# Optimization experiments

Hardware: AMD Instinct MI355X
Metric: run time of the kernel (lower is better)

Reference implementation:

```python
import jax, jax.numpy as jnp
import numpy as np

B, L, D, V, C = 16384, 50, 128, 91718, 11
H, HD, F = 4, 32, 6
NP = F * (F - 1) // 2  # 15 pairs
CIN = F * D + NP * D   # 2688


def setup_inputs() -> dict:
    key = jax.random.key(0)
    ks = jax.random.split(key, 32)
    inp = {}
    inp['item_id'] = jax.random.randint(ks[0], (B,), 0, V)
    inp['item_mm'] = jax.random.normal(ks[1], (B, D), dtype=jnp.float32)
    inp['likes'] = jax.random.randint(ks[2], (B,), 0, C)
    inp['views'] = jax.random.randint(ks[3], (B,), 0, C)
    inp['item_seq'] = jax.random.randint(ks[4], (B, L), 0, V)
    g = lambda k, shape, s: (jax.random.normal(k, shape, dtype=jnp.float32) * s)
    inp['item_emb'] = g(ks[5], (V, D), 0.02).at[0].set(0.0)  # padding_idx=0
    inp['cate_emb'] = g(ks[6], (C, D), 0.02)
    inp['mm_w'] = g(ks[7], (D, D), (2.0 / D) ** 0.5)
    inp['mm_b'] = jnp.zeros((D,), jnp.float32)
    inp['ln_g'] = jnp.ones((D,), jnp.float32)
    inp['ln_b'] = jnp.zeros((D,), jnp.float32)
    inp['gnn_W'] = g(ks[8], (H, D, HD), (2.0 / (D + HD)) ** 0.5 * 1.414)
    inp['gnn_a'] = g(ks[9], (H, 2 * HD, 1), 0.1)
    inp['se_w1'] = g(ks[10], (F, F // 2), 0.4)
    inp['se_b1'] = jnp.zeros((F // 2,), jnp.float32)
    inp['se_w2'] = g(ks[11], (F // 2, F), 0.4)
    inp['se_b2'] = jnp.zeros((F,), jnp.float32)
    inp['bi_W'] = g(ks[12], (F - 1, D, D), (2.0 / (2 * D)) ** 0.5)
    inp['mlp_w1'] = g(ks[13], (CIN, 512), (2.0 / CIN) ** 0.5)
    inp['mlp_b1'] = jnp.zeros((512,), jnp.float32)
    inp['bn1_g'] = jnp.ones((512,), jnp.float32)
    inp['bn1_b'] = jnp.zeros((512,), jnp.float32)
    inp['mlp_w2'] = g(ks[14], (512, 256), (2.0 / 512) ** 0.5)
    inp['mlp_b2'] = jnp.zeros((256,), jnp.float32)
    inp['bn2_g'] = jnp.ones((256,), jnp.float32)
    inp['bn2_b'] = jnp.zeros((256,), jnp.float32)
    inp['mlp_w3'] = g(ks[15], (256, 1), (2.0 / 256) ** 0.5)
    inp['mlp_b3'] = jnp.zeros((1,), jnp.float32)
    return inp


def _forward(item_id, item_mm, likes, views, item_seq,
             item_emb, cate_emb, mm_w, mm_b, ln_g, ln_b,
             gnn_W, gnn_a, se_w1, se_b1, se_w2, se_b2, bi_W,
             mlp_w1, mlp_b1, bn1_g, bn1_b, mlp_w2, mlp_b2, bn2_g, bn2_b,
             mlp_w3, mlp_b3):
    bsz = item_id.shape[0]
    eps = 1e-5

    user_feat = jnp.zeros((bsz, D), item_mm.dtype)
    like_feat = cate_emb[likes]
    view_feat = cate_emb[views]
    id_feat = item_emb[item_id]

    # mm_proj: Linear -> LayerNorm -> GELU (exact)
    y = item_mm @ mm_w + mm_b
    mu = y.mean(-1, keepdims=True)
    var = y.var(-1, keepdims=True)
    y = (y - mu) * jax.lax.rsqrt(var + eps) * ln_g + ln_b
    img_feat = jax.nn.gelu(y, approximate=False)

    # masked mean pooling of history
    seq_emb = item_emb[item_seq]                          # [B,L,D]
    mask = item_seq == 0
    seq_emb = jnp.where(mask[..., None], 0.0, seq_emb)
    cnt = jnp.clip(jnp.sum((~mask).astype(seq_emb.dtype), axis=1, keepdims=True), 1.0)
    hist_feat = seq_emb.sum(1) / cnt

    x = jnp.stack([user_feat, like_feat, view_feat, id_feat, img_feat, hist_feat], axis=1)  # [B,6,D]

    # GAT over 6-node fully-connected feature graph
    hp = jnp.einsum('bni,hio->bnho', x, gnn_W)            # [B,6,H,HD]
    a1 = gnn_a[:, :HD, 0]                                  # [H,HD]
    a2 = gnn_a[:, HD:, 0]
    ei = jnp.einsum('bnhd,hd->bhn', hp, a1)
    ej = jnp.einsum('bnhd,hd->bhn', hp, a2)
    e = ei[:, :, :, None] + ej[:, :, None, :]             # [B,H,6,6]
    e = jnp.where(e > 0, e, 0.2 * e)                       # LeakyReLU(0.2)
    att = jax.nn.softmax(e, axis=-1)                       # dropout off (eval)
    h_new = jnp.einsum('bhnm,bmho->bnho', att, hp).reshape(bsz, F, D)
    gnn_feat = jax.nn.elu(h_new + x)                       # in_dim == out_dim

    # SENet
    z = gnn_feat.mean(-1)                                  # [B,6]
    w = jax.nn.sigmoid(jax.nn.relu(z @ se_w1 + se_b1) @ se_w2 + se_b2)
    s = gnn_feat * w[..., None]

    # Bilinear ('each'): vid_i = s_i @ W_i, pairs (i,j), j>i
    vid = jnp.einsum('bfd,fde->bfe', s[:, :F - 1], bi_W)   # [B,5,D]
    p = jnp.stack([vid[:, i] * s[:, j] for i in range(F - 1) for j in range(i + 1, F)], axis=1)  # [B,15,D]

    c = jnp.concatenate([gnn_feat.reshape(bsz, -1), p.reshape(bsz, -1)], axis=1)  # [B,2688]

    # MLP with eval-mode BatchNorm (running mean 0, var 1) and dropout off
    bn = lambda t, g_, b_: t * (g_ / jnp.sqrt(1.0 + eps)) + b_
    h1 = jax.nn.gelu(bn(c @ mlp_w1 + mlp_b1, bn1_g, bn1_b), approximate=False)
    h2 = jax.nn.gelu(bn(h1 @ mlp_w2 + mlp_b2, bn2_g, bn2_b), approximate=False)
    out = jax.nn.sigmoid(h2 @ mlp_w3 + mlp_b3)
    return out.squeeze(-1)


def reference(item_id, item_mm, likes, views, item_seq,
              item_emb, cate_emb, mm_w, mm_b, ln_g, ln_b,
              gnn_W, gnn_a, se_w1, se_b1, se_w2, se_b2, bi_W,
              mlp_w1, mlp_b1, bn1_g, bn1_b, mlp_w2, mlp_b2, bn2_g, bn2_b,
              mlp_w3, mlp_b3):
    return _forward(item_id, item_mm, likes, views, item_seq,
                    item_emb, cate_emb, mm_w, mm_b, ln_g, ln_b,
                    gnn_W, gnn_a, se_w1, se_b1, se_w2, se_b2, bi_W,
                    mlp_w1, mlp_b1, bn1_g, bn1_b, mlp_w2, mlp_b2, bn2_g, bn2_b,
                    mlp_w3, mlp_b3)
```

## Files before the change

### kernel.cpp

```cpp
#include <hip/hip_runtime.h>
#include <hip/hip_bf16.h>
#include <cstdint>
#include <cstddef>

#define BB 16384

typedef float  floatx4 __attribute__((ext_vector_type(4)));
typedef float  floatx2 __attribute__((ext_vector_type(2)));
typedef __bf16 bf16x8  __attribute__((ext_vector_type(8)));

__device__ __forceinline__ unsigned short f2bf(float f) {
  union { float f; unsigned int u; } v; v.f = f;
  unsigned int r = v.u + 0x7FFFu + ((v.u >> 16) & 1u);
  return (unsigned short)(r >> 16);
}
__device__ __forceinline__ float bf2f(unsigned short h) {
  union { unsigned int u; float f; } v; v.u = ((unsigned int)h) << 16;
  return v.f;
}
__device__ __forceinline__ float gelu_exact(float x) {
  return 0.5f * x * (1.0f + erff(x * 0.7071067811865475f));
}
__device__ __forceinline__ void fp8x8_to_f32(uint2 v, float* o) {
  floatx2 p0 = __builtin_amdgcn_cvt_pk_f32_fp8((int)v.x, false);
  floatx2 p1 = __builtin_amdgcn_cvt_pk_f32_fp8((int)v.x, true);
  floatx2 p2 = __builtin_amdgcn_cvt_pk_f32_fp8((int)v.y, false);
  floatx2 p3 = __builtin_amdgcn_cvt_pk_f32_fp8((int)v.y, true);
  o[0] = p0.x; o[1] = p0.y; o[2] = p1.x; o[3] = p1.y;
  o[4] = p2.x; o[5] = p2.y; o[6] = p3.x; o[7] = p3.y;
}

#define ALOAD16(g, l) \
  __builtin_amdgcn_global_load_lds((const __attribute__((address_space(1))) void*)(g), \
                                   (__attribute__((address_space(3))) void*)(l), 16, 0, 0)

__global__ __launch_bounds__(256)
void k_prep(const float* __restrict__ gnn_W, const float* __restrict__ gnn_a,
            const float* __restrict__ item_mm, const float* __restrict__ item_emb,
            const float* __restrict__ w1, const float* __restrict__ w2,
            const float* __restrict__ bi_W, const float* __restrict__ mm_w,
            unsigned short* __restrict__ wallt2, unsigned short* __restrict__ immb,
            unsigned char* __restrict__ iembf8,
            unsigned short* __restrict__ w1t, unsigned short* __restrict__ w2t,
            unsigned short* __restrict__ biwt, unsigned short* __restrict__ mmwt)
{
  __shared__ float tile[64][65];
  if (blockIdx.x < 2048) {
    const int total = 18432 + 524288 + 1467488;
    for (int id = blockIdx.x * 256 + threadIdx.x; id < total; id += 2048 * 256) {
      if (id < 18432) {
        int n = id / 128, k = id % 128;
        if (n < 128) {
          wallt2[id] = f2bf(gnn_W[(n >> 5) * 4096 + k * 32 + (n & 31)]);
        } else if (n < 136) {
          int h = (n - 128) & 3;
          int off = (n < 132) ? 0 : 32;
          float s = 0.f;
          for (int o = 0; o < 32; o++)
            s += gnn_W[h * 4096 + k * 32 + o] * gnn_a[h * 64 + off + o];
          wallt2[id] = f2bf(s);
        } else {
          wallt2[id] = 0;
        }
      } else if (id < 542720) {
        int l = id - 18432;
        float4 v = ((const float4*)item_mm)[l];
        ushort4 o; o.x = f2bf(v.x); o.y = f2bf(v.y); o.z = f2bf(v.z); o.w = f2bf(v.w);
        ((ushort4*)immb)[l] = o;
      } else {
        int l = id - 542720;
        const float4 v0 = ((const float4*)item_emb)[l * 2];
        const float4 v1 = ((const float4*)item_emb)[l * 2 + 1];
        int lo = __builtin_amdgcn_cvt_pk_fp8_f32(v0.x, v0.y, 0, false);
        lo     = __builtin_amdgcn_cvt_pk_fp8_f32(v0.z, v0.w, lo, true);
        int hi = __builtin_amdgcn_cvt_pk_fp8_f32(v1.x, v1.y, 0, false);
        hi     = __builtin_amdgcn_cvt_pk_fp8_f32(v1.z, v1.w, hi, true);
        uint2 o; o.x = (unsigned int)lo; o.y = (unsigned int)hi;
        ((uint2*)iembf8)[l] = o;
      }
    }
  } else {
    int blk = blockIdx.x - 2048;
    const float* in; unsigned short* outp; int R, C, bx, by;
    if (blk < 336)      { in = w1; outp = w1t; R = 2688; C = 512; bx = blk % 8; by = blk / 8; }
    else if (blk < 368) { blk -= 336; in = w2; outp = w2t; R = 512; C = 256; bx = blk % 4; by = blk / 4; }
    else if (blk < 388) { blk -= 368; int f = blk / 4; int r2 = blk % 4;
                          in = bi_W + f * 16384; outp = biwt + f * 16384;
                          R = 128; C = 128; bx = r2 % 2; by = r2 / 2; }
    else                { blk -= 388; in = mm_w; outp = mmwt; R = 128; C = 128;
                          bx = blk % 2; by = blk / 2; }
    const int c0 = bx * 64, r0 = by * 64;
    const int lr = threadIdx.x >> 6;
    const int lc = threadIdx.x & 63;
    #pragma unroll
    for (int i = 0; i < 16; i++) {
      int r = lr + i * 4;
      tile[r][lc] = in[(size_t)(r0 + r) * C + c0 + lc];
    }
    __syncthreads();
    #pragma unroll
    for (int i = 0; i < 16; i++) {
      int c = lr + i * 4;
      outp[(size_t)(c0 + c) * R + r0 + lc] = f2bf(tile[lc][c]);
    }
  }
}

__global__ __launch_bounds__(512)
void k_featmm(const int* __restrict__ item_id, const int* __restrict__ likes,
              const int* __restrict__ views, const int* __restrict__ item_seq,
              const unsigned char* __restrict__ iembf8, const float* __restrict__ cate_emb,
              const unsigned short* __restrict__ immb, const unsigned short* __restrict__ mmwt,
              const float* __restrict__ mm_b, const float* __restrict__ ln_g,
              const float* __restrict__ ln_b, unsigned short* __restrict__ xb)
{
  __shared__ __align__(16) char smem[64 * 130 * 4];
  const int t = threadIdx.x, lane = t & 63, w = t >> 6;

  if (blockIdx.x < 2048) {
    const int b = blockIdx.x * 8 + w;
    const int g = lane >> 4, l16 = lane & 15;
    const size_t base = (size_t)b * 768;
    const int li = likes[b], vi = views[b], id = item_id[b];

    const int ng = (g < 2) ? 13 : 12;
    int idxs[13];
    #pragma unroll
    for (int e = 0; e < 13; e++)
      idxs[e] = (e < ng) ? item_seq[b * 50 + g + 4 * e] : 0;

    float acc[8] = {0.f, 0.f, 0.f, 0.f, 0.f, 0.f, 0.f, 0.f};
    float cnt = 0.f;
    #pragma unroll
    for (int e = 0; e < 13; e++) {
      const int idx = idxs[e];
      if (idx != 0) {
        cnt += 1.0f;
        uint2 v = *(const uint2*)&iembf8[(size_t)idx * 128 + l16 * 8];
        float dv[8];
        fp8x8_to_f32(v, dv);
        #pragma unroll
        for (int k = 0; k < 8; k++) acc[k] += dv[k];
      }
    }
    #pragma unroll
    for (int k = 0; k < 8; k++) {
      acc[k] += __shfl_xor(acc[k], 16, 64);
      acc[k] += __shfl_xor(acc[k], 32, 64);
    }
    cnt += __shfl_xor(cnt, 16, 64);
    cnt += __shfl_xor(cnt, 32, 64);
    const float ic = 1.0f / fmaxf(cnt, 1.0f);

    *(unsigned int*)&xb[base + lane * 2] = 0u;

    if (g == 0) {
      uint4 o;
      o.x = (unsigned int)f2bf(acc[0] * ic) | ((unsigned int)f2bf(acc[1] * ic) << 16);
      o.y = (unsigned int)f2bf(acc[2] * ic) | ((unsigned int)f2bf(acc[3] * ic) << 16);
      o.z = (unsigned int)f2bf(acc[4] * ic) | ((unsigned int)f2bf(acc[5] * ic) << 16);
      o.w = (unsigned int)f2bf(acc[6] * ic) | ((unsigned int)f2bf(acc[7] * ic) << 16);
      *(uint4*)&xb[base + 640 + l16 * 8] = o;
    } else if (g == 1) {
      uint2 v = *(const uint2*)&iembf8[(size_t)id * 128 + l16 * 8];
      float dv[8];
      fp8x8_to_f32(v, dv);
      uint4 o;
      o.x = (unsigned int)f2bf(dv[0]) | ((unsigned int)f2bf(dv[1]) << 16);
      o.y = (unsigned int)f2bf(dv[2]) | ((unsigned int)f2bf(dv[3]) << 16);
      o.z = (unsigned int)f2bf(dv[4]) | ((unsigned int)f2bf(dv[5]) << 16);
      o.w = (unsigned int)f2bf(dv[6]) | ((unsigned int)f2bf(dv[7]) << 16);
      *(uint4*)&xb[base + 384 + l16 * 8] = o;
    } else {
      const int ci = (g == 2) ? li : vi;
      const float4 v0 = *(const float4*)&cate_emb[(size_t)ci * 128 + l16 * 8];
      const float4 v1 = *(const float4*)&cate_emb[(size_t)ci * 128 + l16 * 8 + 4];
      uint4 o;
      o.x = (unsigned int)f2bf(v0.x) | ((unsigned int)f2bf(v0.y) << 16);
      o.y = (unsigned int)f2bf(v0.z) | ((unsigned int)f2bf(v0.w) << 16);
      o.z = (unsigned int)f2bf(v1.x) | ((unsigned int)f2bf(v1.y) << 16);
      o.w = (unsigned int)f2bf(v1.z) | ((unsigned int)f2bf(v1.w) << 16);
      *(uint4*)&xb[base + 128 + (g - 2) * 128 + l16 * 8] = o;
    }
    return;
  }

  unsigned short* As = (unsigned short*)smem;
  unsigned short* Bs = (unsigned short*)(smem + 8192);
  float* cls = (float*)smem;

  const int lr = lane & 15, lq = lane >> 4;
  const int m0 = (blockIdx.x - 2048) * 64;

  floatx4 acc[4];
  #pragma unroll
  for (int a = 0; a < 4; a++) acc[a] = (floatx4){0.f, 0.f, 0.f, 0.f};

  const int srow = lane >> 3;
  const int schk = (lane & 7) ^ srow;
  const int rb0 = w * 24;

  for (int k0 = 0; k0 < 128; k0 += 64) {
    __syncthreads();
    #pragma unroll
    for (int q = 0; q < 3; q++) {
      const int rb = rb0 + q * 8;
      if (rb < 64) ALOAD16(immb + (size_t)(m0 + rb + srow) * 128 + k0 + schk * 8, As + rb * 64);
      else { const int rbb = rb - 64; ALOAD16(mmwt + (size_t)(rbb + srow) * 128 + k0 + schk * 8, Bs + rbb * 64); }
    }
    __syncthreads();
    #pragma unroll
    for (int ko = 0; ko < 2; ko++) {
      bf16x8 af[4], bv;
      #pragma unroll
      for (int mt = 0; mt < 4; mt++) {
        const int row = mt * 16 + lr;
        const int pc = (ko * 4 + lq) ^ (lr & 7);
        af[mt] = __builtin_bit_cast(bf16x8, *(const uint4*)&As[row * 64 + pc * 8]);
      }
      {
        const int row = w * 16 + lr;
        const int pc = (ko * 4 + lq) ^ (lr & 7);
        bv = __builtin_bit_cast(bf16x8, *(const uint4*)&Bs[row * 64 + pc * 8]);
      }
      #pragma unroll
      for (int mt = 0; mt < 4; mt++)
        acc[mt] = __builtin_amdgcn_mfma_f32_16x16x32_bf16(af[mt], bv, acc[mt], 0, 0, 0);
    }
  }

  __syncthreads();
  #pragma unroll
  for (int mt = 0; mt < 4; mt++)
    #pragma unroll
    for (int i = 0; i < 4; i++) {
      const int rr = mt * 16 + lq * 4 + i;
      const int cc = w * 16 + lr;
      cls[rr * 130 + cc] = acc[mt][i] + mm_b[cc];
    }
  __syncthreads();

  const float2 g2 = *(const float2*)&ln_g[lane * 2];
  const float2 b2 = *(const float2*)&ln_b[lane * 2];
  #pragma unroll
  for (int rr = 0; rr < 8; rr++) {
    const int r = w * 8 + rr;
    float2 v = *(const float2*)&cls[r * 130 + lane * 2];
    float s = v.x + v.y, s2 = v.x * v.x + v.y * v.y;
    #pragma unroll
    for (int o = 32; o > 0; o >>= 1) { s += __shfl_xor(s, o, 64); s2 += __shfl_xor(s2, o, 64); }
    float mu  = s * (1.0f / 128.0f);
    float var = s2 * (1.0f / 128.0f) - mu * mu;
    float rs  = rsqrtf(var + 1e-5f);
    float t0 = gelu_exact((v.x - mu) * rs * g2.x + b2.x);
    float t1 = gelu_exact((v.y - mu) * rs * g2.y + b2.y);
    unsigned int pk = (unsigned int)f2bf(t0) | ((unsigned int)f2bf(t1) << 16);
    *(unsigned int*)&xb[(size_t)(m0 + r) * 768 + 512 + lane * 2] = pk;
  }
}

__global__ __launch_bounds__(512)
void gemm_mlp1(const unsigned short* __restrict__ A, const unsigned short* __restrict__ Bt,
               unsigned short* __restrict__ Cp,
               const float* __restrict__ bias, const float* __restrict__ bng,
               const float* __restrict__ bnb)
{
  int p = blockIdx.y * gridDim.x + blockIdx.x;
  int xcd = p & 7, slot = p >> 3;
  const int bx = slot % gridDim.x;
  const int by = xcd * (gridDim.y >> 3) + slot / gridDim.x;
  const int n0 = bx * 128;
  const int m0 = by * 128;

  __shared__ __align__(16) unsigned short As[128 * 64];
  __shared__ __align__(16) unsigned short Bs[128 * 64];
  const int t = threadIdx.x, lane = t & 63, w = t >> 6;
  const int wm = w & 1, wn = w >> 1;
  const int lr = lane & 15, lq = lane >> 4;

  floatx4 acc[4][2];
  #pragma unroll
  for (int a = 0; a < 4; a++)
    #pragma unroll
    for (int b = 0; b < 2; b++) acc[a][b] = (floatx4){0.f, 0.f, 0.f, 0.f};

  const int srow = lane >> 3;
  const int schk = (lane & 7) ^ srow;
  const int rb0 = w * 32;

  for (int k0 = 0; k0 < 2688; k0 += 64) {
    __syncthreads();
    #pragma unroll
    for (int q = 0; q < 4; q++) {
      const int rb = rb0 + q * 8;
      if (rb < 128) {
        ALOAD16(A + (size_t)(m0 + rb + srow) * 2688 + k0 + schk * 8, As + rb * 64);
      } else {
        ALOAD16(Bt + (size_t)(n0 + rb - 128 + srow) * 2688 + k0 + schk * 8, Bs + (rb - 128) * 64);
      }
    }
    __syncthreads();
    #pragma unroll
    for (int ko = 0; ko < 2; ko++) {
      bf16x8 af[4], bfv[2];
      #pragma unroll
      for (int mt = 0; mt < 4; mt++) {
        const int row = wm * 64 + mt * 16 + lr;
        const int pc = (ko * 4 + lq) ^ (lr & 7);
        af[mt] = __builtin_bit_cast(bf16x8, *(const uint4*)&As[row * 64 + pc * 8]);
      }
      #pragma unroll
      for (int nt = 0; nt < 2; nt++) {
        const int row = wn * 32 + nt * 16 + lr;
        const int pc = (ko * 4 + lq) ^ (lr & 7);
        bfv[nt] = __builtin_bit_cast(bf16x8, *(const uint4*)&Bs[row * 64 + pc * 8]);
      }
      #pragma unroll
      for (int mt = 0; mt < 4; mt++)
        #pragma unroll
        for (int nt = 0; nt < 2; nt++)
          acc[mt][nt] = __builtin_amdgcn_mfma_f32_16x16x32_bf16(af[mt], bfv[nt], acc[mt][nt], 0, 0, 0);
    }
  }

  #pragma unroll
  for (int mt = 0; mt < 4; mt++)
    #pragma unroll
    for (int nt = 0; nt < 2; nt++)
      #pragma unroll
      for (int i = 0; i < 4; i++) {
        const int cm = m0 + wm * 64 + mt * 16 + lq * 4 + i;
        const int cn = n0 + wn * 32 + nt * 16 + lr;
        float tt = acc[mt][nt][i] + bias[cn];
        tt = tt * (bng[cn] * 0.9999950000374997f) + bnb[cn];
        Cp[(size_t)cm * 512 + cn] = f2bf(gelu_exact(tt));
      }
}

__global__ __launch_bounds__(256)
void k_hpatt(const unsigned short* __restrict__ xb, const unsigned short* __restrict__ wallt2,
             const float* __restrict__ se_w1, const float* __restrict__ se_b1,
             const float* __restrict__ se_w2, const float* __restrict__ se_b2,
             unsigned short* __restrict__ c, unsigned short* __restrict__ sb)
{
  __shared__ __align__(16) char smem[30720];
  unsigned short* As = (unsigned short*)smem;
  unsigned short* Bs = (unsigned short*)(smem + 12288);
  unsigned short* hps = (unsigned short*)smem;

  const int t = threadIdx.x, lane = t & 63, w = t >> 6;
  const int wm = w & 1, wn = w >> 1;
  const int lr = lane & 15, lq = lane >> 4;
  const int m0 = blockIdx.x * 96;

  floatx4 acc[3][5];
  #pragma unroll
  for (int a = 0; a < 3; a++)
    #pragma unroll
    for (int b = 0; b < 5; b++) acc[a][b] = (floatx4){0.f, 0.f, 0.f, 0.f};

  const int srow = lane >> 3;
  const int schk = (lane & 7) ^ srow;

  for (int k0 = 0; k0 < 128; k0 += 64) {
    __syncthreads();
    #pragma unroll
    for (int q = 0; q < 8; q++) {
      const int e = w + 4 * q;
      if (e < 30) {
        const int rb = e * 8;
        if (rb < 96) {
          ALOAD16(xb + (size_t)(m0 + rb + srow) * 128 + k0 + schk * 8, As + rb * 64);
        } else {
          const int rbb = rb - 96;
          ALOAD16(wallt2 + (size_t)(rbb + srow) * 128 + k0 + schk * 8, Bs + rbb * 64);
        }
      }
    }
    __syncthreads();
    #pragma unroll
    for (int ko = 0; ko < 2; ko++) {
      bf16x8 af[3];
      #pragma unroll
      for (int mt = 0; mt < 3; mt++) {
        const int row = wm * 48 + mt * 16 + lr;
        const int pc = (ko * 4 + lq) ^ (lr & 7);
        af[mt] = __builtin_bit_cast(bf16x8, *(const uint4*)&As[row * 64 + pc * 8]);
      }
      #pragma unroll
      for (int nt = 0; nt < 5; nt++) {
        if (nt < 4 || wn == 0) {
          const int tid = wn + 2 * nt;
          const int row = tid * 16 + lr;
          const int pc = (ko * 4 + lq) ^ (lr & 7);
          bf16x8 bfv = __builtin_bit_cast(bf16x8, *(const uint4*)&Bs[row * 64 + pc * 8]);
          #pragma unroll
          for (int mt = 0; mt < 3; mt++)
            acc[mt][nt] = __builtin_amdgcn_mfma_f32_16x16x32_bf16(af[mt], bfv, acc[mt][nt], 0, 0, 0);
        }
      }
    }
  }

  __syncthreads();
  #pragma unroll
  for (int mt = 0; mt < 3; mt++)
    #pragma unroll
    for (int nt = 0; nt < 5; nt++)
      if (nt < 4 || wn == 0) {
        const int tid = wn + 2 * nt;
        #pragma unroll
        for (int i = 0; i < 4; i++) {
          const int rr = wm * 48 + mt * 16 + lq * 4 + i;
          const int cc = tid * 16 + lr;
          hps[rr * 146 + cc] = f2bf(acc[mt][nt][i]);
        }
      }
  __syncthreads();

  const int hh = lane >> 4;

  for (int it = 0; it < 4; it++) {
    const int lb = w * 4 + it;
    const int b = blockIdx.x * 16 + lb;
    const unsigned short* hb = hps + lb * 6 * 146;

    float2 vm[6];
    float ein[6], ejn[6];
    #pragma unroll
    for (int m = 0; m < 6; m++) {
      unsigned int pk = *(const unsigned int*)&hb[m * 146 + lane * 2];
      vm[m].x = bf2f((unsigned short)(pk & 0xFFFFu));
      vm[m].y = bf2f((unsigned short)(pk >> 16));
      ein[m] = bf2f(hb[m * 146 + 128 + hh]);
      ejn[m] = bf2f(hb[m * 146 + 132 + hh]);
    }

    float g0[6], g1[6], zz[6];
    #pragma unroll
    for (int n = 0; n < 6; n++) {
      float ev[6]; float mx = -1e30f;
      #pragma unroll
      for (int m = 0; m < 6; m++) {
        float e = ein[n] + ejn[m];
        e = e > 0.f ? e : 0.2f * e;
        ev[m] = e; mx = fmaxf(mx, e);
      }
      float ss = 0.f;
      #pragma unroll
      for (int m = 0; m < 6; m++) { ev[m] = __expf(ev[m] - mx); ss += ev[m]; }
      const float inv = 1.0f / ss;
      float hn0 = 0.f, hn1 = 0.f;
      #pragma unroll
      for (int m = 0; m < 6; m++) {
        const float a = ev[m] * inv;
        hn0 += a * vm[m].x; hn1 += a * vm[m].y;
      }
      unsigned int xp = *(const unsigned int*)&xb[(size_t)b * 768 + n * 128 + lane * 2];
      float A0 = hn0 + bf2f((unsigned short)(xp & 0xFFFFu));
      float A1 = hn1 + bf2f((unsigned short)(xp >> 16));
      A0 = A0 > 0.f ? A0 : __expf(A0) - 1.0f;
      A1 = A1 > 0.f ? A1 : __expf(A1) - 1.0f;
      g0[n] = A0; g1[n] = A1;
      float zacc = A0 + A1;
      #pragma unroll
      for (int o = 32; o > 0; o >>= 1) zacc += __shfl_xor(zacc, o, 64);
      zz[n] = zacc * (1.0f / 128.0f);
    }

    float rr3[3];
    #pragma unroll
    for (int j = 0; j < 3; j++) {
      float a = se_b1[j];
      #pragma unroll
      for (int n = 0; n < 6; n++) a += zz[n] * se_w1[n * 3 + j];
      rr3[j] = fmaxf(a, 0.f);
    }
    float wse[6];
    #pragma unroll
    for (int n = 0; n < 6; n++) {
      float a = se_b2[n];
      #pragma unroll
      for (int j = 0; j < 3; j++) a += rr3[j] * se_w2[j * 6 + n];
      wse[n] = 1.0f / (1.0f + __expf(-a));
    }

    #pragma unroll
    for (int n = 0; n < 6; n++) {
      unsigned int pc = (unsigned int)f2bf(g0[n]) | ((unsigned int)f2bf(g1[n]) << 16);
      unsigned int ps = (unsigned int)f2bf(g0[n] * wse[n]) | ((unsigned int)f2bf(g1[n] * wse[n]) << 16);
      *(unsigned int*)&c[(size_t)b * 2688 + n * 128 + lane * 2]  = pc;
      *(unsigned int*)&sb[(size_t)b * 768 + n * 128 + lane * 2]  = ps;
    }
  }
}

__global__ __launch_bounds__(256)
void gemm_vid(const unsigned short* __restrict__ sbb, const unsigned short* __restrict__ biwt,
              unsigned short* __restrict__ c)
{
  const int z = blockIdx.z;
  const int m0 = blockIdx.y * 128;
  __shared__ __align__(16) unsigned short smem[128 * 130];
  unsigned short* As = smem;
  unsigned short* Bs = smem + 8192;
  const int t = threadIdx.x;
  const int lane = t & 63, w = t >> 6;
  const int wm = w & 1, wn = w >> 1;
  const int lr = lane & 15, lq = lane >> 4;

  floatx4 acc[4][4];
  #pragma unroll
  for (int a = 0; a < 4; a++)
    #pragma unroll
    for (int b = 0; b < 4; b++) acc[a][b] = (floatx4){0.f, 0.f, 0.f, 0.f};

  const int srow = lane >> 3;
  const int schk = (lane & 7) ^ srow;
  const unsigned short* Ag = sbb + (size_t)(m0 + w * 32 + srow) * 768 + z * 128 + schk * 8;
  const unsigned short* Bg = biwt + z * 16384 + (size_t)(w * 32 + srow) * 128 + schk * 8;
  unsigned short* AsW = As + w * 32 * 64;
  unsigned short* BsW = Bs + w * 32 * 64;

  for (int k0 = 0; k0 < 128; k0 += 64) {
    __syncthreads();
    #pragma unroll
    for (int q = 0; q < 4; q++) {
      ALOAD16(Ag + k0 + (size_t)(q * 8) * 768, AsW + q * 512);
      ALOAD16(Bg + k0 + (size_t)(q * 8) * 128, BsW + q * 512);
    }
    __syncthreads();
    #pragma unroll
    for (int ko = 0; ko < 2; ko++) {
      bf16x8 af[4], bfv[4];
      #pragma unroll
      for (int mt = 0; mt < 4; mt++) {
        const int row = wm * 64 + mt * 16 + lr;
        const int pc = (ko * 4 + lq) ^ (lr & 7);
        af[mt] = __builtin_bit_cast(bf16x8, *(const uint4*)&As[row * 64 + pc * 8]);
      }
      #pragma unroll
      for (int nt = 0; nt < 4; nt++) {
        const int row = wn * 64 + nt * 16 + lr;
        const int pc = (ko * 4 + lq) ^ (lr & 7);
        bfv[nt] = __builtin_bit_cast(bf16x8, *(const uint4*)&Bs[row * 64 + pc * 8]);
      }
      #pragma unroll
      for (int mt = 0; mt < 4; mt++)
        #pragma unroll
        for (int nt = 0; nt < 4; nt++)
          acc[mt][nt] = __builtin_amdgcn_mfma_f32_16x16x32_bf16(af[mt], bfv[nt], acc[mt][nt], 0, 0, 0);
    }
  }

  __syncthreads();
  #pragma unroll
  for (int mt = 0; mt < 4; mt++)
    #pragma unroll
    for (int nt = 0; nt < 4; nt++)
      #pragma unroll
      for (int i = 0; i < 4; i++) {
        const int rr = wm * 64 + mt * 16 + lq * 4 + i;
        const int cc = wn * 64 + nt * 16 + lr;
        smem[rr * 130 + cc] = f2bf(acc[mt][nt][i]);
      }
  __syncthreads();

  const int pb0[5] = {0, 5, 9, 12, 14};
  const int npairs = 5 - z;
  const int tot = 128 * 32 * npairs;
  for (int e = t; e < tot; e += 256) {
    const int g  = e & 31;
    const int rp = e >> 5;
    const int p  = rp % npairs;
    const int r  = rp / npairs;
    ushort4 vv = *(const ushort4*)&smem[r * 130 + g * 4];
    ushort4 sv = *(const ushort4*)&sbb[(size_t)(m0 + r) * 768 + (z + 1 + p) * 128 + g * 4];
    ushort4 o;
    o.x = f2bf(bf2f(vv.x) * bf2f(sv.x));
    o.y = f2bf(bf2f(vv.y) * bf2f(sv.y));
    o.z = f2bf(bf2f(vv.z) * bf2f(sv.z));
    o.w = f2bf(bf2f(vv.w) * bf2f(sv.w));
    *(ushort4*)&c[(size_t)(m0 + r) * 2688 + 768 + (size_t)(pb0[z] + p) * 128 + g * 4] = o;
  }
}

__global__ __launch_bounds__(512)
void k_mlp2out(const unsigned short* __restrict__ A, const unsigned short* __restrict__ Bt,
               const float* __restrict__ b2v, const float* __restrict__ bng,
               const float* __restrict__ bnb, const float* __restrict__ w3,
               const float* __restrict__ b3, float* __restrict__ out)
{
  __shared__ __align__(16) char smem[40960];
  unsigned short* As = (unsigned short*)smem;
  unsigned short* Bs = (unsigned short*)(smem + 8192);
  unsigned short* h2s = (unsigned short*)smem;

  const int t = threadIdx.x, lane = t & 63, w = t >> 6;
  const int lr = lane & 15, lq = lane >> 4;
  const int m0 = blockIdx.x * 64;

  floatx4 acc[4][2];
  #pragma unroll
  for (int a = 0; a < 4; a++)
    #pragma unroll
    for (int b = 0; b < 2; b++) acc[a][b] = (floatx4){0.f, 0.f, 0.f, 0.f};

  const int srow = lane >> 3;
  const int schk = (lane & 7) ^ srow;
  const int rb0 = w * 40;

  for (int k0 = 0; k0 < 512; k0 += 64) {
    __syncthreads();
    #pragma unroll
    for (int q = 0; q < 5; q++) {
      const int rb = rb0 + q * 8;
      if (rb < 64) ALOAD16(A + (size_t)(m0 + rb + srow) * 512 + k0 + schk * 8, As + rb * 64);
      else { const int rbb = rb - 64; ALOAD16(Bt + (size_t)(rbb + srow) * 512 + k0 + schk * 8, Bs + rbb * 64); }
    }
    __syncthreads();
    #pragma unroll
    for (int ko = 0; ko < 2; ko++) {
      bf16x8 af[4], bfv[2];
      #pragma unroll
      for (int mt = 0; mt < 4; mt++) {
        const int row = mt * 16 + lr;
        const int pc = (ko * 4 + lq) ^ (lr & 7);
        af[mt] = __builtin_bit_cast(bf16x8, *(const uint4*)&As[row * 64 + pc * 8]);
      }
      #pragma unroll
      for (int nt = 0; nt < 2; nt++) {
        const int row = w * 32 + nt * 16 + lr;
        const int pc = (ko * 4 + lq) ^ (lr & 7);
        bfv[nt] = __builtin_bit_cast(bf16x8, *(const uint4*)&Bs[row * 64 + pc * 8]);
      }
      #pragma unroll
      for (int mt = 0; mt < 4; mt++)
        #pragma unroll
        for (int nt = 0; nt < 2; nt++)
          acc[mt][nt] = __builtin_amdgcn_mfma_f32_16x16x32_bf16(af[mt], bfv[nt], acc[mt][nt], 0, 0, 0);
    }
  }

  __syncthreads();
  #pragma unroll
  for (int mt = 0; mt < 4; mt++)
    #pragma unroll
    for (int nt = 0; nt < 2; nt++)
      #pragma unroll
      for (int i = 0; i < 4; i++) {
        const int rr = mt * 16 + lq * 4 + i;
        const int cc = w * 32 + nt * 16 + lr;
        float tt = acc[mt][nt][i] + b2v[cc];
        tt = tt * (bng[cc] * 0.9999950000374997f) + bnb[cc];
        h2s[rr * 264 + cc] = f2bf(gelu_exact(tt));
      }
  __syncthreads();

  const float4 w4 = *(const float4*)&w3[lane * 4];
  #pragma unroll
  for (int rr = 0; rr < 8; rr++) {
    const int r = w * 8 + rr;
    ushort4 v = *(const ushort4*)&h2s[r * 264 + lane * 4];
    float a = bf2f(v.x) * w4.x + bf2f(v.y) * w4.y + bf2f(v.z) * w4.z + bf2f(v.w) * w4.w;
    #pragma unroll
    for (int o = 32; o > 0; o >>= 1) a += __shfl_xor(a, o, 64);
    if (lane == 0) out[m0 + r] = 1.0f / (1.0f + __expf(-(a + b3[0])));
  }
}

#define OFF_MMWT   0ull
#define OFF_BIWT   65536ull
#define OFF_W1T    229376ull
#define OFF_W2T    2981888ull
#define OFF_IMMB   3244032ull
#define OFF_XB     7438336ull
#define OFF_SB     57769984ull
#define OFF_C      82935808ull
#define OFF_IEMB   179404800ull
#define OFF_WALLT2 191144704ull

extern "C" void kernel_launch(void* const* d_in, const int* in_sizes, int n_in,
                              void* d_out, int out_size, void* d_ws, size_t ws_size,
                              hipStream_t stream)
{
  const int*   item_id  = (const int*)  d_in[0];
  const float* item_mm  = (const float*)d_in[1];
  const int*   likes    = (const int*)  d_in[2];
  const int*   views    = (const int*)  d_in[3];
  const int*   item_seq = (const int*)  d_in[4];
  const float* item_emb = (const float*)d_in[5];
  const float* cate_emb = (const float*)d_in[6];
  const float* mm_w     = (const float*)d_in[7];
  const float* mm_b     = (const float*)d_in[8];
  const float* ln_g     = (const float*)d_in[9];
  const float* ln_b     = (const float*)d_in[10];
  const float* gnn_W    = (const float*)d_in[11];
  const float* gnn_a    = (const float*)d_in[12];
  const float* se_w1    = (const float*)d_in[13];
  const float* se_b1    = (const float*)d_in[14];
  const float* se_w2    = (const float*)d_in[15];
  const float* se_b2    = (const float*)d_in[16];
  const float* bi_W     = (const float*)d_in[17];
  const float* mlp_w1   = (const float*)d_in[18];
  const float* mlp_b1   = (const float*)d_in[19];
  const float* bn1_g    = (const float*)d_in[20];
  const float* bn1_b    = (const float*)d_in[21];
  const float* mlp_w2   = (const float*)d_in[22];
  const float* mlp_b2   = (const float*)d_in[23];
  const float* bn2_g    = (const float*)d_in[24];
  const float* bn2_b    = (const float*)d_in[25];
  const float* mlp_w3   = (const float*)d_in[26];
  const float* mlp_b3   = (const float*)d_in[27];
  float* out = (float*)d_out;

  char* ws = (char*)d_ws;
  unsigned short* mmwt   = (unsigned short*)(ws + OFF_MMWT);
  unsigned short* biwt   = (unsigned short*)(ws + OFF_BIWT);
  unsigned short* w1t    = (unsigned short*)(ws + OFF_W1T);
  unsigned short* w2t    = (unsigned short*)(ws + OFF_W2T);
  unsigned short* immb   = (unsigned short*)(ws + OFF_IMMB);
  unsigned short* xb     = (unsigned short*)(ws + OFF_XB);
  unsigned short* sbb    = (unsigned short*)(ws + OFF_SB);
  unsigned short* cbuf   = (unsigned short*)(ws + OFF_C);
  unsigned short* h1b    = (unsigned short*)(ws + OFF_XB);
  unsigned char*  iembf8 = (unsigned char*) (ws + OFF_IEMB);
  unsigned short* wallt2 = (unsigned short*)(ws + OFF_WALLT2);

  k_prep<<<2440, 256, 0, stream>>>(gnn_W, gnn_a, item_mm, item_emb,
                                   mlp_w1, mlp_w2, bi_W, mm_w,
                                   wallt2, immb, iembf8, w1t, w2t, biwt, mmwt);
  k_featmm<<<2304, 512, 0, stream>>>(item_id, likes, views, item_seq, iembf8, cate_emb,
                                     immb, mmwt, mm_b, ln_g, ln_b, xb);
  k_hpatt<<<1024, 256, 0, stream>>>(xb, wallt2, se_w1, se_b1, se_w2, se_b2, cbuf, sbb);
  gemm_vid<<<dim3(1, 128, 5), 256, 0, stream>>>(sbb, biwt, cbuf);
  gemm_mlp1<<<dim3(4, 128), 512, 0, stream>>>(cbuf, w1t, h1b, mlp_b1, bn1_g, bn1_b);
  k_mlp2out<<<256, 512, 0, stream>>>(h1b, w2t, mlp_b2, bn2_g, bn2_b, mlp_w3, mlp_b3, out);
}
```

Baseline: 320.6 us.

## Triple-buffer MLP1 GEMM with 128x256 tiles and interleaved async loads

```diff
diff --git a/kernel.cpp b/kernel.cpp
--- a/kernel.cpp
+++ b/kernel.cpp
@@ -259,83 +259,131 @@
   }
 }
 
-__global__ __launch_bounds__(512)
+
+#define MLP1_PHASE(As_, Bs_, KO, NTB, LOADA, JS, JN, TST, STB, EW)             \
+  {                                                                            \
+    if (LOADA) {                                                               \
+      _Pragma("unroll")                                                        \
+      for (int mt = 0; mt < 4; mt++) {                                         \
+        const int row = wm * 64 + mt * 16 + lr;                                \
+        const int pc = ((KO) * 4 + lq) ^ (lr & 7);                             \
+        af[mt] = __builtin_bit_cast(bf16x8, *(const uint4*)&(As_)[row * 64 + pc * 8]); \
+      }                                                                        \
+    }                                                                          \
+    bf16x8 bv0, bv1;                                                           \
+    {                                                                          \
+      const int pc = ((KO) * 4 + lq) ^ (lr & 7);                               \
+      const int r0 = wn * 64 + (NTB) * 16 + lr;                                \
+      bv0 = __builtin_bit_cast(bf16x8, *(const uint4*)&(Bs_)[r0 * 64 + pc * 8]); \
+      bv1 = __builtin_bit_cast(bf16x8, *(const uint4*)&(Bs_)[(r0 + 16) * 64 + pc * 8]); \
+    }                                                                          \
+    _Pragma("unroll")                                                          \
+    for (int j = 0; j < (JN); j++)                                             \
+      ALOAD16(gsrc[(JS) + j] + (size_t)(TST) * 64, (STB) + ldst[(JS) + j]);    \
+    __builtin_amdgcn_s_barrier();                                              \
+    asm volatile("s_waitcnt lgkmcnt(0)");                                      \
+    __builtin_amdgcn_s_setprio(1);                                             \
+    _Pragma("unroll")                                                          \
+    for (int mt = 0; mt < 4; mt++) {                                           \
+      acc[mt][(NTB)]     = __builtin_amdgcn_mfma_f32_16x16x32_bf16(af[mt], bv0, acc[mt][(NTB)], 0, 0, 0);     \
+      acc[mt][(NTB) + 1] = __builtin_amdgcn_mfma_f32_16x16x32_bf16(af[mt], bv1, acc[mt][(NTB) + 1], 0, 0, 0); \
+    }                                                                          \
+    __builtin_amdgcn_s_setprio(0);                                             \
+    if ((EW) == 1) asm volatile("s_waitcnt vmcnt(6)" ::: "memory");            \
+    if ((EW) == 2) asm volatile("s_waitcnt vmcnt(0)" ::: "memory");            \
+    __builtin_amdgcn_s_barrier();                                              \
+  }
+
+#define MLP1_TILE(TT, SB, STB, NST, EW)                                        \
+  {                                                                            \
+    const unsigned short* As_ = (SB);                                          \
+    const unsigned short* Bs_ = (SB) + 8192;                                   \
+    MLP1_PHASE(As_, Bs_, 0, 0, 1, 0, (NST) ? 2 : 0, (TT) + 2, (STB), 0)        \
+    MLP1_PHASE(As_, Bs_, 0, 2, 0, 2, (NST) ? 2 : 0, (TT) + 2, (STB), 0)        \
+    MLP1_PHASE(As_, Bs_, 1, 0, 1, 4, (NST) ? 1 : 0, (TT) + 2, (STB), 0)        \
+    MLP1_PHASE(As_, Bs_, 1, 2, 0, 5, (NST) ? 1 : 0, (TT) + 2, (STB), (EW))     \
+  }
+
+__global__ __launch_bounds__(512, 2)
 void gemm_mlp1(const unsigned short* __restrict__ A, const unsigned short* __restrict__ Bt,
                unsigned short* __restrict__ Cp,
                const float* __restrict__ bias, const float* __restrict__ bng,
                const float* __restrict__ bnb)
 {
-  int p = blockIdx.y * gridDim.x + blockIdx.x;
-  int xcd = p & 7, slot = p >> 3;
-  const int bx = slot % gridDim.x;
-  const int by = xcd * (gridDim.y >> 3) + slot / gridDim.x;
-  const int n0 = bx * 128;
-  const int m0 = by * 128;
-
-  __shared__ __align__(16) unsigned short As[128 * 64];
-  __shared__ __align__(16) unsigned short Bs[128 * 64];
+  __shared__ __align__(16) unsigned short lds[3 * 24576];
+
   const int t = threadIdx.x, lane = t & 63, w = t >> 6;
   const int wm = w & 1, wn = w >> 1;
   const int lr = lane & 15, lq = lane >> 4;
 
-  floatx4 acc[4][2];
+  const int p = blockIdx.x;
+  const int xcd = p & 7, sl = p >> 3;
+  const int by = xcd * 16 + (sl >> 1);
+  const int bx = sl & 1;
+  const int m0 = by * 128, n0 = bx * 256;
+
+  floatx4 acc[4][4];
   #pragma unroll
   for (int a = 0; a < 4; a++)
     #pragma unroll
-    for (int b = 0; b < 2; b++) acc[a][b] = (floatx4){0.f, 0.f, 0.f, 0.f};
+    for (int b = 0; b < 4; b++) acc[a][b] = (floatx4){0.f, 0.f, 0.f, 0.f};
 
   const int srow = lane >> 3;
   const int schk = (lane & 7) ^ srow;
-  const int rb0 = w * 32;
-
-  for (int k0 = 0; k0 < 2688; k0 += 64) {
-    __syncthreads();
-    #pragma unroll
-    for (int q = 0; q < 4; q++) {
-      const int rb = rb0 + q * 8;
-      if (rb < 128) {
-        ALOAD16(A + (size_t)(m0 + rb + srow) * 2688 + k0 + schk * 8, As + rb * 64);
-      } else {
-        ALOAD16(Bt + (size_t)(n0 + rb - 128 + srow) * 2688 + k0 + schk * 8, Bs + (rb - 128) * 64);
-      }
-    }
-    __syncthreads();
-    #pragma unroll
-    for (int ko = 0; ko < 2; ko++) {
-      bf16x8 af[4], bfv[2];
-      #pragma unroll
-      for (int mt = 0; mt < 4; mt++) {
-        const int row = wm * 64 + mt * 16 + lr;
-        const int pc = (ko * 4 + lq) ^ (lr & 7);
-        af[mt] = __builtin_bit_cast(bf16x8, *(const uint4*)&As[row * 64 + pc * 8]);
-      }
-      #pragma unroll
-      for (int nt = 0; nt < 2; nt++) {
-        const int row = wn * 32 + nt * 16 + lr;
-        const int pc = (ko * 4 + lq) ^ (lr & 7);
-        bfv[nt] = __builtin_bit_cast(bf16x8, *(const uint4*)&Bs[row * 64 + pc * 8]);
-      }
-      #pragma unroll
-      for (int mt = 0; mt < 4; mt++)
-        #pragma unroll
-        for (int nt = 0; nt < 2; nt++)
-          acc[mt][nt] = __builtin_amdgcn_mfma_f32_16x16x32_bf16(af[mt], bfv[nt], acc[mt][nt], 0, 0, 0);
-    }
-  }
+
+  const unsigned short* gsrc[6];
+  unsigned int ldst[6];
+  #pragma unroll
+  for (int j = 0; j < 6; j++) {
+    const int e = w * 6 + j;
+    if (e < 16) {
+      gsrc[j] = A + (size_t)(m0 + e * 8 + srow) * 2688 + schk * 8;
+      ldst[j] = e * 512u;
+    } else {
+      gsrc[j] = Bt + (size_t)(n0 + (e - 16) * 8 + srow) * 2688 + schk * 8;
+      ldst[j] = 8192u + (e - 16) * 512u;
+    }
+  }
+
+  unsigned short* s0 = lds;
+  unsigned short* s1 = lds + 24576;
+  unsigned short* s2 = lds + 2 * 24576;
+
+  bf16x8 af[4];
+
+  #pragma unroll
+  for (int j = 0; j < 6; j++) ALOAD16(gsrc[j], s0 + ldst[j]);
+  #pragma unroll
+  for (int j = 0; j < 6; j++) ALOAD16(gsrc[j] + 64, s1 + ldst[j]);
+  asm volatile("s_waitcnt vmcnt(6)" ::: "memory");
+  __builtin_amdgcn_s_barrier();
+
+  for (int it = 0; it < 13; it++) {
+    const int tt = it * 3;
+    MLP1_TILE(tt,     s0, s2, 6, 1)
+    MLP1_TILE(tt + 1, s1, s0, 6, 1)
+    MLP1_TILE(tt + 2, s2, s1, 6, 1)
+  }
+  MLP1_TILE(39, s0, s2, 6, 1)
+  MLP1_TILE(40, s1, s0, 0, 2)
+  MLP1_TILE(41, s2, s1, 0, 0)
 
   #pragma unroll
   for (int mt = 0; mt < 4; mt++)
     #pragma unroll
-    for (int nt = 0; nt < 2; nt++)
+    for (int nt = 0; nt < 4; nt++)
       #pragma unroll
       for (int i = 0; i < 4; i++) {
         const int cm = m0 + wm * 64 + mt * 16 + lq * 4 + i;
-        const int cn = n0 + wn * 32 + nt * 16 + lr;
-        float tt = acc[mt][nt][i] + bias[cn];
-        tt = tt * (bng[cn] * 0.9999950000374997f) + bnb[cn];
-        Cp[(size_t)cm * 512 + cn] = f2bf(gelu_exact(tt));
-      }
-}
+        const int cn = n0 + wn * 64 + nt * 16 + lr;
+        float tv = acc[mt][nt][i] + bias[cn];
+        tv = tv * (bng[cn] * 0.9999950000374997f) + bnb[cn];
+        Cp[(size_t)cm * 512 + cn] = f2bf(gelu_exact(tv));
+      }
+}
+
+#undef MLP1_TILE
+#undef MLP1_PHASE
 
 __global__ __launch_bounds__(256)
 void k_hpatt(const unsigned short* __restrict__ xb, const unsigned short* __restrict__ wallt2,
@@ -734,6 +782,6 @@
                                      immb, mmwt, mm_b, ln_g, ln_b, xb);
   k_hpatt<<<1024, 256, 0, stream>>>(xb, wallt2, se_w1, se_b1, se_w2, se_b2, cbuf, sbb);
   gemm_vid<<<dim3(1, 128, 5), 256, 0, stream>>>(sbb, biwt, cbuf);
-  gemm_mlp1<<<dim3(4, 128), 512, 0, stream>>>(cbuf, w1t, h1b, mlp_b1, bn1_g, bn1_b);
+  gemm_mlp1<<<256, 512, 0, stream>>>(cbuf, w1t, h1b, mlp_b1, bn1_g, bn1_b);
   k_mlp2out<<<256, 512, 0, stream>>>(h1b, w2t, mlp_b2, bn2_g, bn2_b, mlp_w3, mlp_b3, out);
 }
```

After: 372.8 us. 1.16x slower.
